# Kernel optimization log

Measured on AMD Instinct MI355X. Metric: run time of the kernel, lower is better.

## Reference

```python
import jax, jax.numpy as jnp
import numpy as np

S = 3072        # packed sequence length
DIM = 1280      # hidden size
H = 16          # num heads
HD = DIM // H   # head dim = 80
NSEG = 3        # number of packed segments


def setup_inputs() -> dict:
    key = jax.random.key(0)
    ks = jax.random.split(key, 6)
    hidden_states = jax.random.normal(ks[0], (S, DIM), jnp.float32)
    cos = jax.random.uniform(ks[1], (S, HD), jnp.float32, minval=-1.0, maxval=1.0)
    sin = jax.random.uniform(ks[2], (S, HD), jnp.float32, minval=-1.0, maxval=1.0)
    qkv_w = jax.random.normal(ks[3], (3 * DIM, DIM), jnp.float32) * 0.02
    qkv_b = jnp.zeros((3 * DIM,), jnp.float32)
    proj_w = jax.random.normal(ks[4], (DIM, DIM), jnp.float32) * 0.02
    proj_b = jnp.zeros((DIM,), jnp.float32)
    # 3 equal segments; cu_seqlens = [0, 1024, 2048, 3072]
    cu_seqlens = jnp.arange(NSEG + 1, dtype=jnp.int32) * (S // NSEG)
    return {
        "hidden_states": hidden_states, "cos": cos, "sin": sin,
        "qkv_w": qkv_w, "qkv_b": qkv_b, "proj_w": proj_w, "proj_b": proj_b,
        "cu_seqlens": cu_seqlens,
    }


def rotate_half(x):
    x1, x2 = jnp.split(x, 2, axis=-1)
    return jnp.concatenate((-x2, x1), axis=-1)


def reference(hidden_states, cos, sin, qkv_w, qkv_b, proj_w, proj_b, cu_seqlens):
    seq = hidden_states.shape[0]
    # QKV projection: [S, 3*DIM] -> [S, 3, H, HD]
    qkv = (hidden_states @ qkv_w.T + qkv_b).reshape(seq, 3, H, HD)
    q, k, v = qkv[:, 0], qkv[:, 1], qkv[:, 2]  # each [S, H, HD]
    # RoPE in float32, cos/sin broadcast over heads via [S, 1, HD]
    c = cos[:, None, :].astype(jnp.float32)
    s = sin[:, None, :].astype(jnp.float32)
    qf, kf = q.astype(jnp.float32), k.astype(jnp.float32)
    q = (qf * c + rotate_half(qf) * s).astype(q.dtype)
    k = (kf * c + rotate_half(kf) * s).astype(k.dtype)
    # Block-diagonal additive mask from cu_seqlens (vectorized, no loop)
    pos = jnp.arange(seq)
    seg = jnp.searchsorted(cu_seqlens, pos, side="right")  # segment id per token
    neg = jnp.finfo(jnp.float32).min
    mask = jnp.where(seg[:, None] == seg[None, :], 0.0, neg)  # [S, S]
    # Dense attention over packed sequence
    scores = jnp.einsum("shd,thd->hst", q, k) / np.sqrt(HD).astype(np.float32)
    scores = scores + mask  # broadcast over heads
    attn = jax.nn.softmax(scores.astype(jnp.float32), axis=-1).astype(q.dtype)
    out = jnp.einsum("hst,thd->shd", attn, v).reshape(seq, DIM)
    return out @ proj_w.T + proj_b
```

## Files before the change

### kernel.cpp

```cpp
#include <hip/hip_runtime.h>
#include <hip/hip_bf16.h>


#define S_TOT 3072
#define DIM   1280
#define NH    16
#define HD    80
#define SEG   1024
#define TDIM  3840
#define K1    1280

typedef short v8s __attribute__((ext_vector_type(8)));
typedef float v4f __attribute__((ext_vector_type(4)));

__device__ __forceinline__ short f2bf(float v) {
  __hip_bfloat16 b = __float2bfloat16(v);
  return *reinterpret_cast<short*>(&b);
}

__device__ __forceinline__ float bf2f(short s) {
  unsigned u = ((unsigned)(unsigned short)s) << 16;
  float f;
  __builtin_memcpy(&f, &u, 4);
  return f;
}

__device__ __forceinline__ void gload16(const void* g, void* lds) {
  __builtin_amdgcn_global_load_lds(
      (const __attribute__((address_space(1))) char*)g,
      (__attribute__((address_space(3))) char*)lds, 16, 0, 0);
}

#define CVT_N1 (S_TOT * DIM / 4)
#define CVT_N2 (TDIM * DIM / 4)
#define CVT_N3 (DIM * DIM / 4)
__global__ __launch_bounds__(256) void cvt3(const float* __restrict__ in1,
                                            const float* __restrict__ in2,
                                            const float* __restrict__ in3,
                                            __hip_bfloat16* __restrict__ o1,
                                            __hip_bfloat16* __restrict__ o2,
                                            __hip_bfloat16* __restrict__ o3) {
  int i = blockIdx.x * 256 + threadIdx.x;
  const float* in;
  __hip_bfloat16* out;
  if (i < CVT_N1) { in = in1; out = o1; }
  else if (i < CVT_N1 + CVT_N2) { in = in2; out = o2; i -= CVT_N1; }
  else { in = in3; out = o3; i -= CVT_N1 + CVT_N2; }
  const float4 v = ((const float4*)in)[i];
  __hip_bfloat162 p0, p1;
  p0.x = __float2bfloat16(v.x); p0.y = __float2bfloat16(v.y);
  p1.x = __float2bfloat16(v.z); p1.y = __float2bfloat16(v.w);
  __hip_bfloat162* o = (__hip_bfloat162*)(out + (size_t)i * 4);
  o[0] = p0; o[1] = p1;
}

extern __shared__ short ring[];

__global__ __launch_bounds__(512, 2) void gemm1_3r(const __hip_bfloat16* __restrict__ A,
                                                   const __hip_bfloat16* __restrict__ B,
                                                   const float* __restrict__ bias,
                                                   __hip_bfloat16* __restrict__ C) {
  const int tid  = threadIdx.x;
  const int wave = tid >> 6;
  const int lane = tid & 63;
  const int quad = lane >> 4;
  const int l16  = lane & 15;
  const int wmp  = wave >> 2;
  const int wnp  = wave & 3;
  const int bm = blockIdx.x * 256;
  const int bn = blockIdx.y * 256;

  const int r0 = ((tid >> 3) << 1) + ((tid >> 2) & 1);
  const int gs = (tid & 3) ^ ((tid >> 3) & 3);
  const short* A0 = (const short*)A + (size_t)(bm + r0) * K1 + gs * 8;
  const short* A1 = A0 + (size_t)128 * K1;
  const short* B0 = (const short*)B + (size_t)(bn + r0) * K1 + gs * 8;
  const short* B1 = B0 + (size_t)128 * K1;
  const int wst = wave * 512;

#define STG(sbuf, ko) do {                              \
    short* d_ = ring + (sbuf) * 16384;                  \
    gload16(A0 + (ko), d_ + wst);                       \
    gload16(A1 + (ko), d_ + 4096 + wst);                \
    gload16(B0 + (ko), d_ + 8192 + wst);                \
    gload16(B1 + (ko), d_ + 12288 + wst);               \
  } while (0)

  const int posA  = quad ^ ((l16 >> 1) & 3);
  const int rbase = (l16 >> 1) * 64 + (l16 & 1) * 32 + posA * 8;
  const int Abase = wmp * 4096 + rbase;
  const int Bbase = 8192 + wnp * 2048 + rbase;

  v4f acc[8][4];
  const v4f vz = {0.f, 0.f, 0.f, 0.f};
  #pragma unroll
  for (int i = 0; i < 8; ++i)
    #pragma unroll
    for (int j = 0; j < 4; ++j) acc[i][j] = vz;

  STG(0, 0);
  STG(1, 32);
  asm volatile("s_waitcnt vmcnt(4)" ::: "memory");
  __builtin_amdgcn_s_barrier();
  __builtin_amdgcn_sched_barrier(0);

  int cb = 0, sb = 2;
  for (int t = 0; t < 40; ++t) {
    if (t + 2 < 40) STG(sb, (t + 2) * 32);

    const short* lb = ring + cb * 16384;
    v8s af[8], bf[4];
    #pragma unroll
    for (int i = 0; i < 8; ++i) af[i] = *(const v8s*)&lb[Abase + i * 512];
    #pragma unroll
    for (int j = 0; j < 4; ++j) bf[j] = *(const v8s*)&lb[Bbase + j * 512];

    __builtin_amdgcn_s_setprio(1);
    #pragma unroll
    for (int i = 0; i < 8; ++i)
      #pragma unroll
      for (int j = 0; j < 4; ++j)
        acc[i][j] = __builtin_amdgcn_mfma_f32_16x16x32_bf16(af[i], bf[j], acc[i][j], 0, 0, 0);
    __builtin_amdgcn_s_setprio(0);

    if (t < 39) {
      if (t + 2 < 40) asm volatile("s_waitcnt vmcnt(4)" ::: "memory");
      else            asm volatile("s_waitcnt vmcnt(0)" ::: "memory");
      __builtin_amdgcn_s_barrier();
      __builtin_amdgcn_sched_barrier(0);
    }
    cb = (cb == 2) ? 0 : cb + 1;
    sb = (sb == 2) ? 0 : sb + 1;
  }
#undef STG

  #pragma unroll
  for (int j = 0; j < 4; ++j) {
    const int col = bn + wnp * 64 + j * 16 + l16;
    const float bj = bias[col];
    #pragma unroll
    for (int i = 0; i < 8; ++i) {
      const int row0 = bm + wmp * 128 + i * 16 + quad * 4;
      #pragma unroll
      for (int r = 0; r < 4; ++r)
        C[(size_t)(row0 + r) * TDIM + col] = __float2bfloat16(acc[i][j][r] + bj);
    }
  }
}

__global__ __launch_bounds__(256) void gemm2_c(const __hip_bfloat16* __restrict__ A,
                                               const __hip_bfloat16* __restrict__ B,
                                               const float* __restrict__ bias,
                                               float* __restrict__ C,
                                               int M, int N, int K) {
  __shared__ __align__(16) short Abuf[2][4096];
  __shared__ __align__(16) short Bbuf[2][8192];
  const int tid  = threadIdx.x;
  const int wave = tid >> 6;
  const int lane = tid & 63;
  const int quad = lane >> 4;
  const int l16  = lane & 15;
  const int bm = blockIdx.x * 64;
  const int bn = blockIdx.y * 128;
  const int wm = (wave & 1) * 32;
  const int wn = (wave >> 1) * 64;

  const int srow = tid >> 3;
  const int skh  = tid & 7;
  const __hip_bfloat16* Ag[2];
  const __hip_bfloat16* Bg[4];
  int Ao[2], Bo[4];
  #pragma unroll
  for (int l = 0; l < 2; ++l) {
    const int row = l * 32 + srow;
    Ag[l] = A + (size_t)(bm + row) * K + skh * 8;
    Ao[l] = (row * 8 + (skh ^ (row & 7))) * 8;
  }
  #pragma unroll
  for (int l = 0; l < 4; ++l) {
    const int row = l * 32 + srow;
    Bg[l] = B + (size_t)(bn + row) * K + skh * 8;
    Bo[l] = (row * 8 + (skh ^ (row & 7))) * 8;
  }

  v4f acc[2][4];
  const v4f vz = {0.f, 0.f, 0.f, 0.f};
  #pragma unroll
  for (int i = 0; i < 2; ++i)
    #pragma unroll
    for (int j = 0; j < 4; ++j) acc[i][j] = vz;

  const int sw = l16 & 7;
  const int nk = K >> 6;
  v8s ra[2], rb[4];

  #pragma unroll
  for (int l = 0; l < 2; ++l) ra[l] = *(const v8s*)Ag[l];
  #pragma unroll
  for (int l = 0; l < 4; ++l) rb[l] = *(const v8s*)Bg[l];
  #pragma unroll
  for (int l = 0; l < 2; ++l) *(v8s*)&Abuf[0][Ao[l]] = ra[l];
  #pragma unroll
  for (int l = 0; l < 4; ++l) *(v8s*)&Bbuf[0][Bo[l]] = rb[l];
  __syncthreads();

  for (int k = 0; k < nk; ++k) {
    const int cur = k & 1;
    const bool more = (k + 1 < nk);
    if (more) {
      const int off = (k + 1) * 64;
      #pragma unroll
      for (int l = 0; l < 2; ++l) ra[l] = *(const v8s*)(Ag[l] + off);
      #pragma unroll
      for (int l = 0; l < 4; ++l) rb[l] = *(const v8s*)(Bg[l] + off);
    }
    #pragma unroll
    for (int s = 0; s < 2; ++s) {
      const int khx = (s * 4 + quad) ^ sw;
      v8s af[2], bf[4];
      #pragma unroll
      for (int i = 0; i < 2; ++i)
        af[i] = *(const v8s*)&Abuf[cur][((wm + i * 16 + l16) * 8 + khx) * 8];
      #pragma unroll
      for (int j = 0; j < 4; ++j)
        bf[j] = *(const v8s*)&Bbuf[cur][((wn + j * 16 + l16) * 8 + khx) * 8];
      #pragma unroll
      for (int i = 0; i < 2; ++i)
        #pragma unroll
        for (int j = 0; j < 4; ++j)
          acc[i][j] = __builtin_amdgcn_mfma_f32_16x16x32_bf16(af[i], bf[j], acc[i][j], 0, 0, 0);
    }
    if (more) {
      #pragma unroll
      for (int l = 0; l < 2; ++l) *(v8s*)&Abuf[1 - cur][Ao[l]] = ra[l];
      #pragma unroll
      for (int l = 0; l < 4; ++l) *(v8s*)&Bbuf[1 - cur][Bo[l]] = rb[l];
    }
    __syncthreads();
  }

  #pragma unroll
  for (int j = 0; j < 4; ++j) {
    const int col = bn + wn + j * 16 + l16;
    const float bj = bias[col];
    #pragma unroll
    for (int i = 0; i < 2; ++i) {
      const int row0 = bm + wm + i * 16 + quad * 4;
      #pragma unroll
      for (int r = 0; r < 4; ++r)
        C[(size_t)(row0 + r) * N + col] = acc[i][j][r] + bj;
    }
  }
}

#define QK_BLOCKS ((2 * S_TOT * 16 * 12) / 256)
#define V_BLOCKS  ((3 * 16 * 16 * 8 * 96) / 256)
__global__ __launch_bounds__(256) void pack_all(const __hip_bfloat16* __restrict__ qkv,
                                                const float* __restrict__ cos_,
                                                const float* __restrict__ sin_,
                                                short* __restrict__ Qp,
                                                short* __restrict__ Kp,
                                                short* __restrict__ Vp) {
  const int bid = blockIdx.x;
  if (bid < QK_BLOCKS) {
    const int idx = bid * 256 + threadIdx.x;
    const int kd = idx % 12;
    const int h  = (idx / 12) % 16;
    const int s  = (idx / 192) % S_TOT;
    const int p  = idx / (192 * S_TOT);
    const int seg = s >> 10, tb = (s >> 6) & 15, t = s & 63;
    short* out = (p ? Kp : Qp) +
                 ((size_t)(((seg * 16 + h) * 16 + tb) * 12 + kd) * 64 + t) * 8;
    short tmp[8];
    if (kd >= 10) {
      #pragma unroll
      for (int j = 0; j < 8; ++j) tmp[j] = 0;
      *(int4*)out = *(int4*)tmp;
      return;
    }
    const short* row = (const short*)qkv + (size_t)s * TDIM + p * DIM + h * HD;
    const int d0 = kd * 8;
    const v8s xm = *(const v8s*)(row + d0);
    const v8s xr = *(const v8s*)(row + d0 + ((kd < 5) ? 40 : -40));
    const float sgn = (kd < 5) ? -1.f : 1.f;
    const float scale = (p == 0) ? 0.111803398874989485f : 1.0f;
    #pragma unroll
    for (int j = 0; j < 8; ++j) {
      const int d = d0 + j;
      const float v = (bf2f(xm[j]) * cos_[s * HD + d] +
                       sgn * bf2f(xr[j]) * sin_[s * HD + d]) * scale;
      tmp[j] = f2bf(v);
    }
    *(int4*)out = *(int4*)tmp;
  } else {
    const int idx = (bid - QK_BLOCKS) * 256 + threadIdx.x;
    const int d  = idx % 96;
    const int td = (idx / 96) % 8;
    const int tb = (idx / 768) % 16;
    const int h  = (idx / (768 * 16)) % 16;
    const int seg = idx / (768 * 256);
    const int s0 = seg * SEG + tb * 64 + td * 8;
    const short* q = (const short*)qkv;
    short tmp[8];
    if (d < 80) {
      #pragma unroll
      for (int j = 0; j < 8; ++j)
        tmp[j] = q[(size_t)(s0 + j) * TDIM + 2 * DIM + h * HD + d];
    } else {
      const short fill = (d == 80) ? (short)0x3F80 : (short)0;
      #pragma unroll
      for (int j = 0; j < 8; ++j) tmp[j] = fill;
    }
    *(int4*)(Vp + (size_t)idx * 8) = *(int4*)tmp;
  }
}

__global__ __launch_bounds__(256, 4) void attn_mfma(const short* __restrict__ Qp,
                                                    const short* __restrict__ Kp,
                                                    const short* __restrict__ Vp,
                                                    __hip_bfloat16* __restrict__ out) {
  __shared__ __align__(16) short Ks[64 * 96];
  __shared__ __align__(16) short Vs[64 * 96];
  __shared__ __align__(16) short Ps[4][16 * 68];

  const int l   = blockIdx.x;
  const int xcd = l & 7;
  const int j8  = l >> 3;
  const int g   = xcd * 6 + (j8 >> 4);
  const int qt  = j8 & 15;
  const int h   = g & 15;
  const int seg = g >> 4;
  const int tid  = threadIdx.x;
  const int wave = tid >> 6;
  const int lane = tid & 63;
  const int quad = lane >> 4;
  const int l16  = lane & 15;
  const int sh16 = g;

  const short* Qg = Qp + (size_t)(sh16 * 16 + qt) * 6144;
  const short* Kg = Kp + (size_t)sh16 * 16 * 6144;
  const short* Vg = Vp + (size_t)sh16 * 16 * 6144;

  v8s af[3];
  #pragma unroll
  for (int ks = 0; ks < 3; ++ks)
    af[ks] = *(const v8s*)(Qg + ((ks * 4 + quad) * 64 + wave * 16 + l16) * 8);

  v8s kr[3], vr[3];
  #pragma unroll
  for (int it = 0; it < 3; ++it) {
    const int o = (it * 256 + tid) * 8;
    kr[it] = *(const v8s*)(Kg + o);
    vr[it] = *(const v8s*)(Vg + o);
  }
  #pragma unroll
  for (int it = 0; it < 3; ++it) {
    const int o = (it * 256 + tid) * 8;
    *(v8s*)&Ks[o] = kr[it];
    *(v8s*)&Vs[o] = vr[it];
  }
  __syncthreads();

  v4f o4[6];
  const v4f vz = {0.f, 0.f, 0.f, 0.f};
  #pragma unroll
  for (int n = 0; n < 6; ++n) o4[n] = vz;

  for (int kb = 0; kb < 16; ++kb) {
    const bool more = (kb + 1 < 16);
    if (more) {
      const size_t base = (size_t)(kb + 1) * 6144;
      #pragma unroll
      for (int it = 0; it < 3; ++it) {
        const int o = (it * 256 + tid) * 8;
        kr[it] = *(const v8s*)(Kg + base + o);
        vr[it] = *(const v8s*)(Vg + base + o);
      }
    }

    v4f s4[4];
    #pragma unroll
    for (int j = 0; j < 4; ++j) {
      s4[j] = vz;
      #pragma unroll
      for (int ks = 0; ks < 3; ++ks) {
        const v8s bf = *(const v8s*)&Ks[((ks * 4 + quad) * 64 + j * 16 + l16) * 8];
        s4[j] = __builtin_amdgcn_mfma_f32_16x16x32_bf16(af[ks], bf, s4[j], 0, 0, 0);
      }
    }

    #pragma unroll
    for (int reg = 0; reg < 4; ++reg)
      #pragma unroll
      for (int j = 0; j < 4; ++j)
        Ps[wave][(quad * 4 + reg) * 68 + j * 16 + l16] = f2bf(__expf(s4[j][reg]));

    v8s pa[2];
    #pragma unroll
    for (int kp = 0; kp < 2; ++kp)
      pa[kp] = *(const v8s*)&Ps[wave][l16 * 68 + kp * 32 + quad * 8];
    #pragma unroll
    for (int n = 0; n < 6; ++n) {
      #pragma unroll
      for (int kp = 0; kp < 2; ++kp) {
        const v8s vb = *(const v8s*)&Vs[((kp * 4 + quad) * 96 + n * 16 + l16) * 8];
        o4[n] = __builtin_amdgcn_mfma_f32_16x16x32_bf16(pa[kp], vb, o4[n], 0, 0, 0);
      }
    }

    __syncthreads();
    if (more) {
      #pragma unroll
      for (int it = 0; it < 3; ++it) {
        const int o = (it * 256 + tid) * 8;
        *(v8s*)&Ks[o] = kr[it];
        *(v8s*)&Vs[o] = vr[it];
      }
    }
    __syncthreads();
  }

  float inv[4];
  #pragma unroll
  for (int r = 0; r < 4; ++r)
    inv[r] = 1.f / __shfl(o4[5][r], quad << 4);
  const int row0 = seg * SEG + qt * 64 + wave * 16 + quad * 4;
  #pragma unroll
  for (int n = 0; n < 5; ++n) {
    const int col = h * HD + n * 16 + l16;
    #pragma unroll
    for (int r = 0; r < 4; ++r)
      out[(size_t)(row0 + r) * DIM + col] = __float2bfloat16(o4[n][r] * inv[r]);
  }
}

extern "C" void kernel_launch(void* const* d_in, const int* in_sizes, int n_in,
                              void* d_out, int out_size, void* d_ws, size_t ws_size,
                              hipStream_t stream) {
  (void)in_sizes; (void)n_in; (void)out_size; (void)ws_size;
  const float* hs     = (const float*)d_in[0];
  const float* cosp   = (const float*)d_in[1];
  const float* sinp   = (const float*)d_in[2];
  const float* qkv_w  = (const float*)d_in[3];
  const float* qkv_b  = (const float*)d_in[4];
  const float* proj_w = (const float*)d_in[5];
  const float* proj_b = (const float*)d_in[6];

  float* out_f = (float*)d_out;
  __hip_bfloat16* qkv_b16 = (__hip_bfloat16*)d_ws;
  __hip_bfloat16* hs_b    = qkv_b16 + (size_t)S_TOT * TDIM;
  __hip_bfloat16* qkvw_b  = hs_b + (size_t)S_TOT * DIM;
  __hip_bfloat16* projw_b = qkvw_b + (size_t)TDIM * DIM;
  short* Qp = (short*)qkvw_b;
  short* Kp = (short*)(projw_b + (size_t)DIM * DIM);
  short* Vp = Kp + (size_t)3 * 16 * 16 * 6144;
  __hip_bfloat16* attn_b = hs_b;

  static bool attr_set = false;
  if (!attr_set) {
    hipFuncSetAttribute((const void*)gemm1_3r,
                        hipFuncAttributeMaxDynamicSharedMemorySize, 98304);
    attr_set = true;
  }

  cvt3<<<(CVT_N1 + CVT_N2 + CVT_N3) / 256, 256, 0, stream>>>(
      hs, qkv_w, proj_w, hs_b, qkvw_b, projw_b);

  gemm1_3r<<<dim3(S_TOT / 256, TDIM / 256), 512, 98304, stream>>>(
      hs_b, qkvw_b, qkv_b, qkv_b16);

  pack_all<<<QK_BLOCKS + V_BLOCKS, 256, 0, stream>>>(qkv_b16, cosp, sinp, Qp, Kp, Vp);

  attn_mfma<<<dim3(768), 256, 0, stream>>>(Qp, Kp, Vp, attn_b);

  gemm2_c<<<dim3(S_TOT / 64, DIM / 128), 256, 0, stream>>>(
      attn_b, projw_b, proj_b, out_f, S_TOT, DIM, DIM);
}
```

Baseline: 204.3 us.

## Rewrite output projection GEMM with triple-buffered direct-to-LDS loads and larger tiles

Replaces the double-buffered register-staged projection GEMM with a version that has a three-stage LDS ring filled by direct global-to-LDS loads (gload16). This matches the pipeline already used for the QKV GEMM. The tile grows from 64x128 to 128x128, with each wave holding a 4x4 accumulator block. MFMA issue priority is raised around the compute, and vmcnt waits are placed explicitly. The goal is to overlap memory with compute and raise reuse, at the cost of halving the grid to 240 blocks and using more registers.

Measured after the change: 205.8 us. No clear change (+0.7%).

```diff
diff --git a/kernel.cpp b/kernel.cpp
--- a/kernel.cpp
+++ b/kernel.cpp
@@ -148,107 +148,94 @@
   }
 }
 
-__global__ __launch_bounds__(256) void gemm2_c(const __hip_bfloat16* __restrict__ A,
-                                               const __hip_bfloat16* __restrict__ B,
-                                               const float* __restrict__ bias,
-                                               float* __restrict__ C,
-                                               int M, int N, int K) {
-  __shared__ __align__(16) short Abuf[2][4096];
-  __shared__ __align__(16) short Bbuf[2][8192];
+__global__ __launch_bounds__(256, 3) void gemm2_3r(const __hip_bfloat16* __restrict__ A,
+                                                   const __hip_bfloat16* __restrict__ B,
+                                                   const float* __restrict__ bias,
+                                                   float* __restrict__ C) {
   const int tid  = threadIdx.x;
   const int wave = tid >> 6;
   const int lane = tid & 63;
   const int quad = lane >> 4;
   const int l16  = lane & 15;
-  const int bm = blockIdx.x * 64;
+  const int wmp  = wave >> 1;
+  const int wnp  = wave & 1;
+  const int bm = blockIdx.x * 128;
   const int bn = blockIdx.y * 128;
-  const int wm = (wave & 1) * 32;
-  const int wn = (wave >> 1) * 64;
-
-  const int srow = tid >> 3;
-  const int skh  = tid & 7;
-  const __hip_bfloat16* Ag[2];
-  const __hip_bfloat16* Bg[4];
-  int Ao[2], Bo[4];
-  #pragma unroll
-  for (int l = 0; l < 2; ++l) {
-    const int row = l * 32 + srow;
-    Ag[l] = A + (size_t)(bm + row) * K + skh * 8;
-    Ao[l] = (row * 8 + (skh ^ (row & 7))) * 8;
-  }
-  #pragma unroll
-  for (int l = 0; l < 4; ++l) {
-    const int row = l * 32 + srow;
-    Bg[l] = B + (size_t)(bn + row) * K + skh * 8;
-    Bo[l] = (row * 8 + (skh ^ (row & 7))) * 8;
-  }
-
-  v4f acc[2][4];
+
+  const int r0 = ((tid >> 3) << 1) + ((tid >> 2) & 1);
+  const int gs = (tid & 3) ^ ((tid >> 3) & 3);
+  const short* A0 = (const short*)A + (size_t)(bm + r0) * K1 + gs * 8;
+  const short* A1 = A0 + (size_t)64 * K1;
+  const short* B0 = (const short*)B + (size_t)(bn + r0) * K1 + gs * 8;
+  const short* B1 = B0 + (size_t)64 * K1;
+  const int wst = wave * 512;
+
+#define STG2(sbuf, ko) do {                             \
+    short* d_ = ring + (sbuf) * 8192;                   \
+    gload16(A0 + (ko), d_ + wst);                       \
+    gload16(A1 + (ko), d_ + 2048 + wst);                \
+    gload16(B0 + (ko), d_ + 4096 + wst);                \
+    gload16(B1 + (ko), d_ + 6144 + wst);                \
+  } while (0)
+
+  const int posA  = quad ^ ((l16 >> 1) & 3);
+  const int rbase = (l16 >> 1) * 64 + (l16 & 1) * 32 + posA * 8;
+  const int Abase = wmp * 2048 + rbase;
+  const int Bbase = 4096 + wnp * 2048 + rbase;
+
+  v4f acc[4][4];
   const v4f vz = {0.f, 0.f, 0.f, 0.f};
   #pragma unroll
-  for (int i = 0; i < 2; ++i)
+  for (int i = 0; i < 4; ++i)
     #pragma unroll
     for (int j = 0; j < 4; ++j) acc[i][j] = vz;
 
-  const int sw = l16 & 7;
-  const int nk = K >> 6;
-  v8s ra[2], rb[4];
-
-  #pragma unroll
-  for (int l = 0; l < 2; ++l) ra[l] = *(const v8s*)Ag[l];
-  #pragma unroll
-  for (int l = 0; l < 4; ++l) rb[l] = *(const v8s*)Bg[l];
-  #pragma unroll
-  for (int l = 0; l < 2; ++l) *(v8s*)&Abuf[0][Ao[l]] = ra[l];
-  #pragma unroll
-  for (int l = 0; l < 4; ++l) *(v8s*)&Bbuf[0][Bo[l]] = rb[l];
-  __syncthreads();
-
-  for (int k = 0; k < nk; ++k) {
-    const int cur = k & 1;
-    const bool more = (k + 1 < nk);
-    if (more) {
-      const int off = (k + 1) * 64;
-      #pragma unroll
-      for (int l = 0; l < 2; ++l) ra[l] = *(const v8s*)(Ag[l] + off);
-      #pragma unroll
-      for (int l = 0; l < 4; ++l) rb[l] = *(const v8s*)(Bg[l] + off);
-    }
-    #pragma unroll
-    for (int s = 0; s < 2; ++s) {
-      const int khx = (s * 4 + quad) ^ sw;
-      v8s af[2], bf[4];
-      #pragma unroll
-      for (int i = 0; i < 2; ++i)
-        af[i] = *(const v8s*)&Abuf[cur][((wm + i * 16 + l16) * 8 + khx) * 8];
+  STG2(0, 0);
+  STG2(1, 32);
+  asm volatile("s_waitcnt vmcnt(4)" ::: "memory");
+  __builtin_amdgcn_s_barrier();
+  __builtin_amdgcn_sched_barrier(0);
+
+  int cb = 0, sb = 2;
+  for (int t = 0; t < 40; ++t) {
+    if (t + 2 < 40) STG2(sb, (t + 2) * 32);
+
+    const short* lb = ring + cb * 8192;
+    v8s af[4], bf[4];
+    #pragma unroll
+    for (int i = 0; i < 4; ++i) af[i] = *(const v8s*)&lb[Abase + i * 512];
+    #pragma unroll
+    for (int j = 0; j < 4; ++j) bf[j] = *(const v8s*)&lb[Bbase + j * 512];
+
+    __builtin_amdgcn_s_setprio(1);
+    #pragma unroll
+    for (int i = 0; i < 4; ++i)
       #pragma unroll
       for (int j = 0; j < 4; ++j)
-        bf[j] = *(const v8s*)&Bbuf[cur][((wn + j * 16 + l16) * 8 + khx) * 8];
-      #pragma unroll
-      for (int i = 0; i < 2; ++i)
-        #pragma unroll
-        for (int j = 0; j < 4; ++j)
-          acc[i][j] = __builtin_amdgcn_mfma_f32_16x16x32_bf16(af[i], bf[j], acc[i][j], 0, 0, 0);
-    }
-    if (more) {
-      #pragma unroll
-      for (int l = 0; l < 2; ++l) *(v8s*)&Abuf[1 - cur][Ao[l]] = ra[l];
-      #pragma unroll
-      for (int l = 0; l < 4; ++l) *(v8s*)&Bbuf[1 - cur][Bo[l]] = rb[l];
-    }
-    __syncthreads();
-  }
+        acc[i][j] = __builtin_amdgcn_mfma_f32_16x16x32_bf16(af[i], bf[j], acc[i][j], 0, 0, 0);
+    __builtin_amdgcn_s_setprio(0);
+
+    if (t < 39) {
+      if (t + 2 < 40) asm volatile("s_waitcnt vmcnt(4)" ::: "memory");
+      else            asm volatile("s_waitcnt vmcnt(0)" ::: "memory");
+      __builtin_amdgcn_s_barrier();
+      __builtin_amdgcn_sched_barrier(0);
+    }
+    cb = (cb == 2) ? 0 : cb + 1;
+    sb = (sb == 2) ? 0 : sb + 1;
+  }
+#undef STG2
 
   #pragma unroll
   for (int j = 0; j < 4; ++j) {
-    const int col = bn + wn + j * 16 + l16;
+    const int col = bn + wnp * 64 + j * 16 + l16;
     const float bj = bias[col];
     #pragma unroll
-    for (int i = 0; i < 2; ++i) {
-      const int row0 = bm + wm + i * 16 + quad * 4;
+    for (int i = 0; i < 4; ++i) {
+      const int row0 = bm + wmp * 64 + i * 16 + quad * 4;
       #pragma unroll
       for (int r = 0; r < 4; ++r)
-        C[(size_t)(row0 + r) * N + col] = acc[i][j][r] + bj;
+        C[(size_t)(row0 + r) * DIM + col] = acc[i][j][r] + bj;
     }
   }
 }
@@ -460,6 +447,8 @@
   if (!attr_set) {
     hipFuncSetAttribute((const void*)gemm1_3r,
                         hipFuncAttributeMaxDynamicSharedMemorySize, 98304);
+    hipFuncSetAttribute((const void*)gemm2_3r,
+                        hipFuncAttributeMaxDynamicSharedMemorySize, 49152);
     attr_set = true;
   }
 
@@ -473,6 +462,6 @@
 
   attn_mfma<<<dim3(768), 256, 0, stream>>>(Qp, Kp, Vp, attn_b);
 
-  gemm2_c<<<dim3(S_TOT / 64, DIM / 128), 256, 0, stream>>>(
-      attn_b, projw_b, proj_b, out_f, S_TOT, DIM, DIM);
-}
+  gemm2_3r<<<dim3(S_TOT / 128, DIM / 128), 256, 49152, stream>>>(
+      attn_b, projw_b, proj_b, out_f);
+}
```
